# Optimization experiments

Measured on AMD Instinct MI355X. Metric: run time of the kernel, lower is better.

The kernel has to match this reference:

```python
import jax, jax.numpy as jnp
import numpy as np

NUM_SKILLS = 50000
HIDDEN = 64
B, T = 8192, 1024
EPS = 1e-6


def setup_inputs() -> dict:
    key = jax.random.key(0)
    ks = jax.random.split(key, 8)
    X = jax.random.randint(ks[0], (B,), 0, NUM_SKILLS)
    y = jax.random.randint(ks[1], (B, T), 0, 2, dtype=jnp.int32)
    embed = jax.random.normal(ks[2], (NUM_SKILLS, HIDDEN), jnp.float32)
    bound = 1.0 / np.sqrt(HIDDEN)
    W0 = jax.random.uniform(ks[3], (HIDDEN, HIDDEN), jnp.float32, -bound, bound)
    b0 = jnp.zeros((HIDDEN,), jnp.float32)
    W1 = jax.random.uniform(ks[4], (HIDDEN, HIDDEN), jnp.float32, -bound, bound)
    b1 = jnp.zeros((HIDDEN,), jnp.float32)
    Wout = jax.random.uniform(ks[5], (HIDDEN, 4), jnp.float32, -bound, bound)
    bout = jnp.zeros((4,), jnp.float32)
    return {"X": X, "y": y, "embed": embed, "W0": W0, "b0": b0,
            "W1": W1, "b1": b1, "Wout": Wout, "bout": bout}


def reference(X, y, embed, W0, b0, W1, b1, Wout, bout):
    # Per-student BKT params from embedding + 2-layer MLP + sigmoid, clamped
    h = embed[X]                                   # (B, H)
    h = jax.nn.relu(h @ W0 + b0)
    h = jax.nn.relu(h @ W1 + b1)
    params = jnp.clip(jax.nn.sigmoid(h @ Wout + bout), EPS, 1.0 - EPS)  # (B, 4)
    l, g, s, prior = params[:, 0], params[:, 1], params[:, 2], params[:, 3]

    def step(latent, y_t):
        true_correct = jnp.where(y_t == -1, 0, y_t)
        correct = latent * (1.0 - s) + (1.0 - latent) * g
        k_t1 = latent * (1.0 - s) / correct
        k_t0 = latent * s / (latent * s + (1.0 - latent) * (1.0 - g))
        k_t = jnp.where(true_correct > 0.5, k_t1, k_t0)
        next_latent = jnp.clip(k_t + (1.0 - k_t) * l, EPS, 1.0 - EPS)
        return next_latent, (correct, latent)

    _, (corrects, latents) = jax.lax.scan(step, prior, y.T)  # scan over T
    return corrects.T, latents.T                            # (B, T) each
```

## Files before the change

kernel.cpp:

```cpp
#include <hip/hip_runtime.h>

#define TSTEPS 1024
#define NROWS  8192
#define CLEN   16
#define KEPS   1e-6f

__device__ __forceinline__ float clampP(float x) {
    return fminf(fmaxf(x, KEPS), 1.f - KEPS);
}
__device__ __forceinline__ float sigm(float v) {
    return 1.0f / (1.0f + __expf(-v));
}

__global__ __launch_bounds__(256) void bkt_fused_v7(
    const int* __restrict__ X, const int* __restrict__ y,
    const float* __restrict__ embed,
    const float* __restrict__ W0, const float* __restrict__ b0,
    const float* __restrict__ W1, const float* __restrict__ b1,
    const float* __restrict__ Wout, const float* __restrict__ bout,
    float* __restrict__ out_corr, float* __restrict__ out_lat)
{
    const int lane = threadIdx.x & 63;
    const int wid  = threadIdx.x >> 6;
    const int row  = blockIdx.x * 4 + wid;

    __shared__ float hstage[4][64];
    __shared__ float trbuf[4][2][64 * 17];
    float* hbuf = hstage[wid];
    float* shc  = trbuf[wid][0];
    float* shl  = trbuf[wid][1];

    const int4* yrow = (const int4*)(y + (size_t)row * TSTEPS);
    const int4 vy0 = yrow[0 * 64 + lane];
    const int4 vy1 = yrow[1 * 64 + lane];
    const int4 vy2 = yrow[2 * 64 + lane];
    const int4 vy3 = yrow[3 * 64 + lane];

    const int skill = X[row];
    hbuf[lane] = embed[(size_t)skill * 64 + lane];
    float acc = b0[lane];
    #pragma unroll
    for (int k4 = 0; k4 < 16; ++k4) {
        const float4 e = *(const float4*)&hbuf[k4 * 4];
        acc = fmaf(e.x, W0[(k4 * 4 + 0) * 64 + lane], acc);
        acc = fmaf(e.y, W0[(k4 * 4 + 1) * 64 + lane], acc);
        acc = fmaf(e.z, W0[(k4 * 4 + 2) * 64 + lane], acc);
        acc = fmaf(e.w, W0[(k4 * 4 + 3) * 64 + lane], acc);
    }
    hbuf[lane] = fmaxf(acc, 0.f);
    acc = b1[lane];
    #pragma unroll
    for (int k4 = 0; k4 < 16; ++k4) {
        const float4 e = *(const float4*)&hbuf[k4 * 4];
        acc = fmaf(e.x, W1[(k4 * 4 + 0) * 64 + lane], acc);
        acc = fmaf(e.y, W1[(k4 * 4 + 1) * 64 + lane], acc);
        acc = fmaf(e.z, W1[(k4 * 4 + 2) * 64 + lane], acc);
        acc = fmaf(e.w, W1[(k4 * 4 + 3) * 64 + lane], acc);
    }
    const float h2 = fmaxf(acc, 0.f);

    const float4 wo = ((const float4*)Wout)[lane];
    float p0 = h2 * wo.x, p1 = h2 * wo.y, p2 = h2 * wo.z, p3 = h2 * wo.w;
    #pragma unroll
    for (int off = 32; off >= 1; off >>= 1) {
        p0 += __shfl_xor(p0, off, 64);
        p1 += __shfl_xor(p1, off, 64);
        p2 += __shfl_xor(p2, off, 64);
        p3 += __shfl_xor(p3, off, 64);
    }
    const float4 bo = *(const float4*)bout;
    const float l     = clampP(sigm(p0 + bo.x));
    const float g     = clampP(sigm(p1 + bo.y));
    const float s     = clampP(sigm(p2 + bo.z));
    const float prior = clampP(sigm(p3 + bo.w));

    unsigned long long B_[4][4];
    B_[0][0] = __ballot(vy0.x > 0); B_[0][1] = __ballot(vy0.y > 0);
    B_[0][2] = __ballot(vy0.z > 0); B_[0][3] = __ballot(vy0.w > 0);
    B_[1][0] = __ballot(vy1.x > 0); B_[1][1] = __ballot(vy1.y > 0);
    B_[1][2] = __ballot(vy1.z > 0); B_[1][3] = __ballot(vy1.w > 0);
    B_[2][0] = __ballot(vy2.x > 0); B_[2][1] = __ballot(vy2.y > 0);
    B_[2][2] = __ballot(vy2.z > 0); B_[2][3] = __ballot(vy2.w > 0);
    B_[3][0] = __ballot(vy3.x > 0); B_[3][1] = __ballot(vy3.y > 0);
    B_[3][2] = __ballot(vy3.z > 0); B_[3][3] = __ballot(vy3.w > 0);
    const int jsel  = lane >> 4;
    const int ibase = (lane & 15) * 4;
    unsigned msk = 0;
    #pragma unroll
    for (int e = 0; e < 4; ++e) {
        const unsigned long long be =
            (jsel == 0) ? B_[0][e] : (jsel == 1) ? B_[1][e] :
            (jsel == 2) ? B_[2][e] : B_[3][e];
        const unsigned n  = (unsigned)(be >> ibase) & 0xFu;
        const unsigned sp = (n & 1u) | ((n & 2u) << 3) | ((n & 4u) << 6) | ((n & 8u) << 9);
        msk |= sp << e;
    }

    const float c1 = 1.f - s - g, d1 = g;
    const float e00_1 = fmaf(l, c1, (1.f - l) * (1.f - s));
    const float e01_1 = l * d1;
    const float c0 = s + g - 1.f, d0 = 1.f - g;
    const float e00_0 = fmaf(l, c0, (1.f - l) * s);
    const float e01_0 = l * d0;

    float m00 = 1.f, m01 = 0.f, m10 = 0.f, m11 = 1.f;
    #pragma unroll
    for (int t = 0; t < CLEN; ++t) {
        const bool one = (msk >> t) & 1u;
        const float e00 = one ? e00_1 : e00_0;
        const float e01 = one ? e01_1 : e01_0;
        const float e10 = one ? c1 : c0;
        const float e11 = one ? d1 : d0;
        const float n00 = fmaf(e00, m00, e01 * m10);
        const float n01 = fmaf(e00, m01, e01 * m11);
        const float n10 = fmaf(e10, m00, e11 * m10);
        const float n11 = fmaf(e10, m01, e11 * m11);
        if ((t & 3) == 3) {
            const float inv = __builtin_amdgcn_rcpf(n11);
            m00 = n00 * inv; m01 = n01 * inv; m10 = n10 * inv; m11 = 1.f;
        } else {
            m00 = n00; m01 = n01; m10 = n10; m11 = n11;
        }
    }

    float s00 = m00, s01 = m01, s10 = m10, s11 = m11;
    #pragma unroll
    for (int d = 1; d < 64; d <<= 1) {
        const float t00 = __shfl_up(s00, d, 64);
        const float t01 = __shfl_up(s01, d, 64);
        const float t10 = __shfl_up(s10, d, 64);
        const float t11 = __shfl_up(s11, d, 64);
        if (lane >= d) {
            const float r00 = fmaf(s00, t00, s01 * t10);
            const float r01 = fmaf(s00, t01, s01 * t11);
            const float r10 = fmaf(s10, t00, s11 * t10);
            const float r11 = fmaf(s10, t01, s11 * t11);
            const float inv = __builtin_amdgcn_rcpf(r11);
            s00 = r00 * inv; s01 = r01 * inv; s10 = r10 * inv; s11 = 1.f;
        }
    }
    const float x00 = __shfl_up(s00, 1, 64);
    const float x01 = __shfl_up(s01, 1, 64);
    const float x10 = __shfl_up(s10, 1, 64);
    const float x11 = __shfl_up(s11, 1, 64);
    float L0;
    if (lane == 0) {
        L0 = prior;
    } else {
        const float num = fmaf(x00, prior, x01);
        const float den = fmaf(x10, prior, x11);
        L0 = clampP(num * __builtin_amdgcn_rcpf(den));
    }

    const float a   = 1.f - s;
    const float omg = 1.f - g;
    const float oml = 1.f - l;
    float Lc = L0;
    #pragma unroll
    for (int t = 0; t < CLEN; ++t) {
        const float correct = fmaf(Lc, c1, g);
        const float den0    = fmaf(Lc, c0, omg);
        shc[lane * 17 + t] = correct;
        shl[lane * 17 + t] = Lc;
        const bool one = (msk >> t) & 1u;
        const float den = one ? correct : den0;
        const float num = Lc * (one ? a : s);
        const float k   = num * __builtin_amdgcn_rcpf(den);
        Lc = clampP(fmaf(k, oml, l));
    }

    float* oc = out_corr + (size_t)row * TSTEPS;
    float* ol = out_lat  + (size_t)row * TSTEPS;
    #pragma unroll
    for (int j = 0; j < 4; ++j) {
        const int c    = j * 16 + (lane >> 2);
        const int q    = (lane & 3) * 4;
        const int base = c * 17 + q;
        float4 vc, vl;
        vc.x = shc[base + 0]; vc.y = shc[base + 1]; vc.z = shc[base + 2]; vc.w = shc[base + 3];
        vl.x = shl[base + 0]; vl.y = shl[base + 1]; vl.z = shl[base + 2]; vl.w = shl[base + 3];
        *(float4*)(oc + j * 256 + lane * 4) = vc;
        *(float4*)(ol + j * 256 + lane * 4) = vl;
    }
}

extern "C" void kernel_launch(void* const* d_in, const int* in_sizes, int n_in,
                              void* d_out, int out_size, void* d_ws, size_t ws_size,
                              hipStream_t stream) {
    const int*   X     = (const int*)  d_in[0];
    const int*   y     = (const int*)  d_in[1];
    const float* embed = (const float*)d_in[2];
    const float* W0    = (const float*)d_in[3];
    const float* b0    = (const float*)d_in[4];
    const float* W1    = (const float*)d_in[5];
    const float* b1    = (const float*)d_in[6];
    const float* Wout  = (const float*)d_in[7];
    const float* bout  = (const float*)d_in[8];

    float* out_corr = (float*)d_out;
    float* out_lat  = out_corr + (size_t)NROWS * TSTEPS;

    bkt_fused_v7<<<NROWS / 4, 256, 0, stream>>>(
        X, y, embed, W0, b0, W1, b1, Wout, bout, out_corr, out_lat);
}
```

Measured before the change: 121.7 us.

## Process two rows per wavefront to interleave independent scan chains

Each wavefront now handles two student rows instead of one. The two rows' MLP, matrix-product scan and recurrence steps are interleaved, which gives more instruction-level parallelism and hides the latency of the serial dependency chains. The W0/W1 weight loads are shared across both rows, and the grid is halved to match. In exchange, register pressure rises, the second row's outputs are buffered in registers before reusing the LDS transpose buffer, and there are half as many waves to hide memory latency.

```diff
diff --git a/kernel.cpp b/kernel.cpp
--- a/kernel.cpp
+++ b/kernel.cpp
@@ -12,7 +12,25 @@
     return 1.0f / (1.0f + __expf(-v));
 }
 
-__global__ __launch_bounds__(256) void bkt_fused_v7(
+__device__ __forceinline__ unsigned fold_msk(
+    const unsigned long long B0[4], const unsigned long long B1[4],
+    const unsigned long long B2[4], const unsigned long long B3[4],
+    int jsel, int ibase)
+{
+    unsigned msk = 0;
+    #pragma unroll
+    for (int e = 0; e < 4; ++e) {
+        const unsigned long long be =
+            (jsel == 0) ? B0[e] : (jsel == 1) ? B1[e] :
+            (jsel == 2) ? B2[e] : B3[e];
+        const unsigned n  = (unsigned)(be >> ibase) & 0xFu;
+        const unsigned sp = (n & 1u) | ((n & 2u) << 3) | ((n & 4u) << 6) | ((n & 8u) << 9);
+        msk |= sp << e;
+    }
+    return msk;
+}
+
+__global__ __launch_bounds__(256) void bkt_fused_v8(
     const int* __restrict__ X, const int* __restrict__ y,
     const float* __restrict__ embed,
     const float* __restrict__ W0, const float* __restrict__ b0,
@@ -22,155 +40,250 @@
 {
     const int lane = threadIdx.x & 63;
     const int wid  = threadIdx.x >> 6;
-    const int row  = blockIdx.x * 4 + wid;
-
-    __shared__ float hstage[4][64];
+    const int rowA = blockIdx.x * 8 + wid * 2;
+    const int rowB = rowA + 1;
+
+    __shared__ float hstage[4][2][64];
     __shared__ float trbuf[4][2][64 * 17];
-    float* hbuf = hstage[wid];
-    float* shc  = trbuf[wid][0];
-    float* shl  = trbuf[wid][1];
-
-    const int4* yrow = (const int4*)(y + (size_t)row * TSTEPS);
-    const int4 vy0 = yrow[0 * 64 + lane];
-    const int4 vy1 = yrow[1 * 64 + lane];
-    const int4 vy2 = yrow[2 * 64 + lane];
-    const int4 vy3 = yrow[3 * 64 + lane];
-
-    const int skill = X[row];
-    hbuf[lane] = embed[(size_t)skill * 64 + lane];
-    float acc = b0[lane];
-    #pragma unroll
-    for (int k4 = 0; k4 < 16; ++k4) {
-        const float4 e = *(const float4*)&hbuf[k4 * 4];
-        acc = fmaf(e.x, W0[(k4 * 4 + 0) * 64 + lane], acc);
-        acc = fmaf(e.y, W0[(k4 * 4 + 1) * 64 + lane], acc);
-        acc = fmaf(e.z, W0[(k4 * 4 + 2) * 64 + lane], acc);
-        acc = fmaf(e.w, W0[(k4 * 4 + 3) * 64 + lane], acc);
-    }
-    hbuf[lane] = fmaxf(acc, 0.f);
-    acc = b1[lane];
-    #pragma unroll
-    for (int k4 = 0; k4 < 16; ++k4) {
-        const float4 e = *(const float4*)&hbuf[k4 * 4];
-        acc = fmaf(e.x, W1[(k4 * 4 + 0) * 64 + lane], acc);
-        acc = fmaf(e.y, W1[(k4 * 4 + 1) * 64 + lane], acc);
-        acc = fmaf(e.z, W1[(k4 * 4 + 2) * 64 + lane], acc);
-        acc = fmaf(e.w, W1[(k4 * 4 + 3) * 64 + lane], acc);
-    }
-    const float h2 = fmaxf(acc, 0.f);
-
-    const float4 wo = ((const float4*)Wout)[lane];
-    float p0 = h2 * wo.x, p1 = h2 * wo.y, p2 = h2 * wo.z, p3 = h2 * wo.w;
-    #pragma unroll
-    for (int off = 32; off >= 1; off >>= 1) {
-        p0 += __shfl_xor(p0, off, 64);
-        p1 += __shfl_xor(p1, off, 64);
-        p2 += __shfl_xor(p2, off, 64);
-        p3 += __shfl_xor(p3, off, 64);
-    }
-    const float4 bo = *(const float4*)bout;
-    const float l     = clampP(sigm(p0 + bo.x));
-    const float g     = clampP(sigm(p1 + bo.y));
-    const float s     = clampP(sigm(p2 + bo.z));
-    const float prior = clampP(sigm(p3 + bo.w));
-
-    unsigned long long B_[4][4];
-    B_[0][0] = __ballot(vy0.x > 0); B_[0][1] = __ballot(vy0.y > 0);
-    B_[0][2] = __ballot(vy0.z > 0); B_[0][3] = __ballot(vy0.w > 0);
-    B_[1][0] = __ballot(vy1.x > 0); B_[1][1] = __ballot(vy1.y > 0);
-    B_[1][2] = __ballot(vy1.z > 0); B_[1][3] = __ballot(vy1.w > 0);
-    B_[2][0] = __ballot(vy2.x > 0); B_[2][1] = __ballot(vy2.y > 0);
-    B_[2][2] = __ballot(vy2.z > 0); B_[2][3] = __ballot(vy2.w > 0);
-    B_[3][0] = __ballot(vy3.x > 0); B_[3][1] = __ballot(vy3.y > 0);
-    B_[3][2] = __ballot(vy3.z > 0); B_[3][3] = __ballot(vy3.w > 0);
+    float* hA  = hstage[wid][0];
+    float* hB  = hstage[wid][1];
+    float* shc = trbuf[wid][0];
+    float* shl = trbuf[wid][1];
+
+    const int4* yA = (const int4*)(y + (size_t)rowA * TSTEPS);
+    const int4* yB = (const int4*)(y + (size_t)rowB * TSTEPS);
+    const int4 va0 = yA[0 * 64 + lane], va1 = yA[1 * 64 + lane];
+    const int4 va2 = yA[2 * 64 + lane], va3 = yA[3 * 64 + lane];
+    const int4 vb0 = yB[0 * 64 + lane], vb1 = yB[1 * 64 + lane];
+    const int4 vb2 = yB[2 * 64 + lane], vb3 = yB[3 * 64 + lane];
+
+    const int skA = X[rowA], skB = X[rowB];
+    const float emA = embed[(size_t)skA * 64 + lane];
+    const float emB = embed[(size_t)skB * 64 + lane];
+
     const int jsel  = lane >> 4;
     const int ibase = (lane & 15) * 4;
-    unsigned msk = 0;
-    #pragma unroll
-    for (int e = 0; e < 4; ++e) {
-        const unsigned long long be =
-            (jsel == 0) ? B_[0][e] : (jsel == 1) ? B_[1][e] :
-            (jsel == 2) ? B_[2][e] : B_[3][e];
-        const unsigned n  = (unsigned)(be >> ibase) & 0xFu;
-        const unsigned sp = (n & 1u) | ((n & 2u) << 3) | ((n & 4u) << 6) | ((n & 8u) << 9);
-        msk |= sp << e;
-    }
-
-    const float c1 = 1.f - s - g, d1 = g;
-    const float e00_1 = fmaf(l, c1, (1.f - l) * (1.f - s));
-    const float e01_1 = l * d1;
-    const float c0 = s + g - 1.f, d0 = 1.f - g;
-    const float e00_0 = fmaf(l, c0, (1.f - l) * s);
-    const float e01_0 = l * d0;
-
-    float m00 = 1.f, m01 = 0.f, m10 = 0.f, m11 = 1.f;
+    unsigned mskA, mskB;
+    {
+        unsigned long long A0[4] = { __ballot(va0.x > 0), __ballot(va0.y > 0),
+                                     __ballot(va0.z > 0), __ballot(va0.w > 0) };
+        unsigned long long A1[4] = { __ballot(va1.x > 0), __ballot(va1.y > 0),
+                                     __ballot(va1.z > 0), __ballot(va1.w > 0) };
+        unsigned long long A2[4] = { __ballot(va2.x > 0), __ballot(va2.y > 0),
+                                     __ballot(va2.z > 0), __ballot(va2.w > 0) };
+        unsigned long long A3[4] = { __ballot(va3.x > 0), __ballot(va3.y > 0),
+                                     __ballot(va3.z > 0), __ballot(va3.w > 0) };
+        mskA = fold_msk(A0, A1, A2, A3, jsel, ibase);
+    }
+    {
+        unsigned long long C0[4] = { __ballot(vb0.x > 0), __ballot(vb0.y > 0),
+                                     __ballot(vb0.z > 0), __ballot(vb0.w > 0) };
+        unsigned long long C1[4] = { __ballot(vb1.x > 0), __ballot(vb1.y > 0),
+                                     __ballot(vb1.z > 0), __ballot(vb1.w > 0) };
+        unsigned long long C2[4] = { __ballot(vb2.x > 0), __ballot(vb2.y > 0),
+                                     __ballot(vb2.z > 0), __ballot(vb2.w > 0) };
+        unsigned long long C3[4] = { __ballot(vb3.x > 0), __ballot(vb3.y > 0),
+                                     __ballot(vb3.z > 0), __ballot(vb3.w > 0) };
+        mskB = fold_msk(C0, C1, C2, C3, jsel, ibase);
+    }
+
+    hA[lane] = emA;
+    hB[lane] = emB;
+    float accA = b0[lane], accB = accA;
+    #pragma unroll
+    for (int k4 = 0; k4 < 16; ++k4) {
+        const float4 eA = *(const float4*)&hA[k4 * 4];
+        const float4 eB = *(const float4*)&hB[k4 * 4];
+        const float w0 = W0[(k4 * 4 + 0) * 64 + lane];
+        const float w1 = W0[(k4 * 4 + 1) * 64 + lane];
+        const float w2 = W0[(k4 * 4 + 2) * 64 + lane];
+        const float w3 = W0[(k4 * 4 + 3) * 64 + lane];
+        accA = fmaf(eA.x, w0, accA); accA = fmaf(eA.y, w1, accA);
+        accA = fmaf(eA.z, w2, accA); accA = fmaf(eA.w, w3, accA);
+        accB = fmaf(eB.x, w0, accB); accB = fmaf(eB.y, w1, accB);
+        accB = fmaf(eB.z, w2, accB); accB = fmaf(eB.w, w3, accB);
+    }
+    hA[lane] = fmaxf(accA, 0.f);
+    hB[lane] = fmaxf(accB, 0.f);
+    accA = b1[lane]; accB = accA;
+    #pragma unroll
+    for (int k4 = 0; k4 < 16; ++k4) {
+        const float4 eA = *(const float4*)&hA[k4 * 4];
+        const float4 eB = *(const float4*)&hB[k4 * 4];
+        const float w0 = W1[(k4 * 4 + 0) * 64 + lane];
+        const float w1 = W1[(k4 * 4 + 1) * 64 + lane];
+        const float w2 = W1[(k4 * 4 + 2) * 64 + lane];
+        const float w3 = W1[(k4 * 4 + 3) * 64 + lane];
+        accA = fmaf(eA.x, w0, accA); accA = fmaf(eA.y, w1, accA);
+        accA = fmaf(eA.z, w2, accA); accA = fmaf(eA.w, w3, accA);
+        accB = fmaf(eB.x, w0, accB); accB = fmaf(eB.y, w1, accB);
+        accB = fmaf(eB.z, w2, accB); accB = fmaf(eB.w, w3, accB);
+    }
+    const float h2A = fmaxf(accA, 0.f);
+    const float h2B = fmaxf(accB, 0.f);
+
+    const float4 wo = ((const float4*)Wout)[lane];
+    float pA0 = h2A * wo.x, pA1 = h2A * wo.y, pA2 = h2A * wo.z, pA3 = h2A * wo.w;
+    float pB0 = h2B * wo.x, pB1 = h2B * wo.y, pB2 = h2B * wo.z, pB3 = h2B * wo.w;
+    #pragma unroll
+    for (int off = 32; off >= 1; off >>= 1) {
+        pA0 += __shfl_xor(pA0, off, 64);
+        pA1 += __shfl_xor(pA1, off, 64);
+        pA2 += __shfl_xor(pA2, off, 64);
+        pA3 += __shfl_xor(pA3, off, 64);
+        pB0 += __shfl_xor(pB0, off, 64);
+        pB1 += __shfl_xor(pB1, off, 64);
+        pB2 += __shfl_xor(pB2, off, 64);
+        pB3 += __shfl_xor(pB3, off, 64);
+    }
+    const float4 bo = *(const float4*)bout;
+    const float lA     = clampP(sigm(pA0 + bo.x));
+    const float gA     = clampP(sigm(pA1 + bo.y));
+    const float sA     = clampP(sigm(pA2 + bo.z));
+    const float priorA = clampP(sigm(pA3 + bo.w));
+    const float lB     = clampP(sigm(pB0 + bo.x));
+    const float gB     = clampP(sigm(pB1 + bo.y));
+    const float sB     = clampP(sigm(pB2 + bo.z));
+    const float priorB = clampP(sigm(pB3 + bo.w));
+
+    const float c1A = 1.f - sA - gA, d1A = gA;
+    const float e00_1A = fmaf(lA, c1A, (1.f - lA) * (1.f - sA));
+    const float e01_1A = lA * d1A;
+    const float c0A = sA + gA - 1.f, d0A = 1.f - gA;
+    const float e00_0A = fmaf(lA, c0A, (1.f - lA) * sA);
+    const float e01_0A = lA * d0A;
+
+    const float c1B = 1.f - sB - gB, d1B = gB;
+    const float e00_1B = fmaf(lB, c1B, (1.f - lB) * (1.f - sB));
+    const float e01_1B = lB * d1B;
+    const float c0B = sB + gB - 1.f, d0B = 1.f - gB;
+    const float e00_0B = fmaf(lB, c0B, (1.f - lB) * sB);
+    const float e01_0B = lB * d0B;
+
+    float mA00 = 1.f, mA01 = 0.f, mA10 = 0.f, mA11 = 1.f;
+    float mB00 = 1.f, mB01 = 0.f, mB10 = 0.f, mB11 = 1.f;
     #pragma unroll
     for (int t = 0; t < CLEN; ++t) {
-        const bool one = (msk >> t) & 1u;
-        const float e00 = one ? e00_1 : e00_0;
-        const float e01 = one ? e01_1 : e01_0;
-        const float e10 = one ? c1 : c0;
-        const float e11 = one ? d1 : d0;
-        const float n00 = fmaf(e00, m00, e01 * m10);
-        const float n01 = fmaf(e00, m01, e01 * m11);
-        const float n10 = fmaf(e10, m00, e11 * m10);
-        const float n11 = fmaf(e10, m01, e11 * m11);
-        if ((t & 3) == 3) {
-            const float inv = __builtin_amdgcn_rcpf(n11);
-            m00 = n00 * inv; m01 = n01 * inv; m10 = n10 * inv; m11 = 1.f;
-        } else {
-            m00 = n00; m01 = n01; m10 = n10; m11 = n11;
-        }
-    }
-
-    float s00 = m00, s01 = m01, s10 = m10, s11 = m11;
+        {
+            const bool one = (mskA >> t) & 1u;
+            const float e00 = one ? e00_1A : e00_0A;
+            const float e01 = one ? e01_1A : e01_0A;
+            const float e10 = one ? c1A : c0A;
+            const float e11 = one ? d1A : d0A;
+            const float n00 = fmaf(e00, mA00, e01 * mA10);
+            const float n01 = fmaf(e00, mA01, e01 * mA11);
+            const float n10 = fmaf(e10, mA00, e11 * mA10);
+            const float n11 = fmaf(e10, mA01, e11 * mA11);
+            if ((t & 3) == 3) {
+                const float inv = __builtin_amdgcn_rcpf(n11);
+                mA00 = n00 * inv; mA01 = n01 * inv; mA10 = n10 * inv; mA11 = 1.f;
+            } else {
+                mA00 = n00; mA01 = n01; mA10 = n10; mA11 = n11;
+            }
+        }
+        {
+            const bool one = (mskB >> t) & 1u;
+            const float e00 = one ? e00_1B : e00_0B;
+            const float e01 = one ? e01_1B : e01_0B;
+            const float e10 = one ? c1B : c0B;
+            const float e11 = one ? d1B : d0B;
+            const float n00 = fmaf(e00, mB00, e01 * mB10);
+            const float n01 = fmaf(e00, mB01, e01 * mB11);
+            const float n10 = fmaf(e10, mB00, e11 * mB10);
+            const float n11 = fmaf(e10, mB01, e11 * mB11);
+            if ((t & 3) == 3) {
+                const float inv = __builtin_amdgcn_rcpf(n11);
+                mB00 = n00 * inv; mB01 = n01 * inv; mB10 = n10 * inv; mB11 = 1.f;
+            } else {
+                mB00 = n00; mB01 = n01; mB10 = n10; mB11 = n11;
+            }
+        }
+    }
+
+    float sA00 = mA00, sA01 = mA01, sA10 = mA10, sA11 = mA11;
+    float sB00 = mB00, sB01 = mB01, sB10 = mB10, sB11 = mB11;
     #pragma unroll
     for (int d = 1; d < 64; d <<= 1) {
-        const float t00 = __shfl_up(s00, d, 64);
-        const float t01 = __shfl_up(s01, d, 64);
-        const float t10 = __shfl_up(s10, d, 64);
-        const float t11 = __shfl_up(s11, d, 64);
+        const float tA00 = __shfl_up(sA00, d, 64);
+        const float tA01 = __shfl_up(sA01, d, 64);
+        const float tA10 = __shfl_up(sA10, d, 64);
+        const float tA11 = __shfl_up(sA11, d, 64);
+        const float tB00 = __shfl_up(sB00, d, 64);
+        const float tB01 = __shfl_up(sB01, d, 64);
+        const float tB10 = __shfl_up(sB10, d, 64);
+        const float tB11 = __shfl_up(sB11, d, 64);
         if (lane >= d) {
-            const float r00 = fmaf(s00, t00, s01 * t10);
-            const float r01 = fmaf(s00, t01, s01 * t11);
-            const float r10 = fmaf(s10, t00, s11 * t10);
-            const float r11 = fmaf(s10, t01, s11 * t11);
-            const float inv = __builtin_amdgcn_rcpf(r11);
-            s00 = r00 * inv; s01 = r01 * inv; s10 = r10 * inv; s11 = 1.f;
-        }
-    }
-    const float x00 = __shfl_up(s00, 1, 64);
-    const float x01 = __shfl_up(s01, 1, 64);
-    const float x10 = __shfl_up(s10, 1, 64);
-    const float x11 = __shfl_up(s11, 1, 64);
-    float L0;
+            {
+                const float r00 = fmaf(sA00, tA00, sA01 * tA10);
+                const float r01 = fmaf(sA00, tA01, sA01 * tA11);
+                const float r10 = fmaf(sA10, tA00, sA11 * tA10);
+                const float r11 = fmaf(sA10, tA01, sA11 * tA11);
+                const float inv = __builtin_amdgcn_rcpf(r11);
+                sA00 = r00 * inv; sA01 = r01 * inv; sA10 = r10 * inv; sA11 = 1.f;
+            }
+            {
+                const float r00 = fmaf(sB00, tB00, sB01 * tB10);
+                const float r01 = fmaf(sB00, tB01, sB01 * tB11);
+                const float r10 = fmaf(sB10, tB00, sB11 * tB10);
+                const float r11 = fmaf(sB10, tB01, sB11 * tB11);
+                const float inv = __builtin_amdgcn_rcpf(r11);
+                sB00 = r00 * inv; sB01 = r01 * inv; sB10 = r10 * inv; sB11 = 1.f;
+            }
+        }
+    }
+    const float xA00 = __shfl_up(sA00, 1, 64);
+    const float xA01 = __shfl_up(sA01, 1, 64);
+    const float xA10 = __shfl_up(sA10, 1, 64);
+    const float xA11 = __shfl_up(sA11, 1, 64);
+    const float xB00 = __shfl_up(sB00, 1, 64);
+    const float xB01 = __shfl_up(sB01, 1, 64);
+    const float xB10 = __shfl_up(sB10, 1, 64);
+    const float xB11 = __shfl_up(sB11, 1, 64);
+    float L0A, L0B;
     if (lane == 0) {
-        L0 = prior;
+        L0A = priorA;
+        L0B = priorB;
     } else {
-        const float num = fmaf(x00, prior, x01);
-        const float den = fmaf(x10, prior, x11);
-        L0 = clampP(num * __builtin_amdgcn_rcpf(den));
-    }
-
-    const float a   = 1.f - s;
-    const float omg = 1.f - g;
-    const float oml = 1.f - l;
-    float Lc = L0;
+        const float numA = fmaf(xA00, priorA, xA01);
+        const float denA = fmaf(xA10, priorA, xA11);
+        L0A = clampP(numA * __builtin_amdgcn_rcpf(denA));
+        const float numB = fmaf(xB00, priorB, xB01);
+        const float denB = fmaf(xB10, priorB, xB11);
+        L0B = clampP(numB * __builtin_amdgcn_rcpf(denB));
+    }
+
+    const float aA = 1.f - sA, omgA = 1.f - gA, omlA = 1.f - lA;
+    const float aB = 1.f - sB, omgB = 1.f - gB, omlB = 1.f - lB;
+    float crB[CLEN], ltB[CLEN];
+    float LcA = L0A, LcB = L0B;
     #pragma unroll
     for (int t = 0; t < CLEN; ++t) {
-        const float correct = fmaf(Lc, c1, g);
-        const float den0    = fmaf(Lc, c0, omg);
-        shc[lane * 17 + t] = correct;
-        shl[lane * 17 + t] = Lc;
-        const bool one = (msk >> t) & 1u;
-        const float den = one ? correct : den0;
-        const float num = Lc * (one ? a : s);
-        const float k   = num * __builtin_amdgcn_rcpf(den);
-        Lc = clampP(fmaf(k, oml, l));
-    }
-
-    float* oc = out_corr + (size_t)row * TSTEPS;
-    float* ol = out_lat  + (size_t)row * TSTEPS;
+        {
+            const float correct = fmaf(LcA, c1A, gA);
+            const float den0    = fmaf(LcA, c0A, omgA);
+            shc[lane * 17 + t] = correct;
+            shl[lane * 17 + t] = LcA;
+            const bool one = (mskA >> t) & 1u;
+            const float den = one ? correct : den0;
+            const float num = LcA * (one ? aA : sA);
+            const float k   = num * __builtin_amdgcn_rcpf(den);
+            LcA = clampP(fmaf(k, omlA, lA));
+        }
+        {
+            const float correct = fmaf(LcB, c1B, gB);
+            const float den0    = fmaf(LcB, c0B, omgB);
+            crB[t] = correct;
+            ltB[t] = LcB;
+            const bool one = (mskB >> t) & 1u;
+            const float den = one ? correct : den0;
+            const float num = LcB * (one ? aB : sB);
+            const float k   = num * __builtin_amdgcn_rcpf(den);
+            LcB = clampP(fmaf(k, omlB, lB));
+        }
+    }
+
+    float* ocA = out_corr + (size_t)rowA * TSTEPS;
+    float* olA = out_lat  + (size_t)rowA * TSTEPS;
     #pragma unroll
     for (int j = 0; j < 4; ++j) {
         const int c    = j * 16 + (lane >> 2);
@@ -179,8 +292,27 @@
         float4 vc, vl;
         vc.x = shc[base + 0]; vc.y = shc[base + 1]; vc.z = shc[base + 2]; vc.w = shc[base + 3];
         vl.x = shl[base + 0]; vl.y = shl[base + 1]; vl.z = shl[base + 2]; vl.w = shl[base + 3];
-        *(float4*)(oc + j * 256 + lane * 4) = vc;
-        *(float4*)(ol + j * 256 + lane * 4) = vl;
+        *(float4*)(ocA + j * 256 + lane * 4) = vc;
+        *(float4*)(olA + j * 256 + lane * 4) = vl;
+    }
+
+    #pragma unroll
+    for (int t = 0; t < CLEN; ++t) {
+        shc[lane * 17 + t] = crB[t];
+        shl[lane * 17 + t] = ltB[t];
+    }
+    float* ocB = out_corr + (size_t)rowB * TSTEPS;
+    float* olB = out_lat  + (size_t)rowB * TSTEPS;
+    #pragma unroll
+    for (int j = 0; j < 4; ++j) {
+        const int c    = j * 16 + (lane >> 2);
+        const int q    = (lane & 3) * 4;
+        const int base = c * 17 + q;
+        float4 vc, vl;
+        vc.x = shc[base + 0]; vc.y = shc[base + 1]; vc.z = shc[base + 2]; vc.w = shc[base + 3];
+        vl.x = shl[base + 0]; vl.y = shl[base + 1]; vl.z = shl[base + 2]; vl.w = shl[base + 3];
+        *(float4*)(ocB + j * 256 + lane * 4) = vc;
+        *(float4*)(olB + j * 256 + lane * 4) = vl;
     }
 }
 
@@ -200,6 +332,6 @@
     float* out_corr = (float*)d_out;
     float* out_lat  = out_corr + (size_t)NROWS * TSTEPS;
 
-    bkt_fused_v7<<<NROWS / 4, 256, 0, stream>>>(
+    bkt_fused_v8<<<NROWS / 8, 256, 0, stream>>>(
         X, y, embed, W0, b0, W1, b1, Wout, bout, out_corr, out_lat);
 }
```

Measured after the change: 119.6 us, median of 2. Within noise of the previous version (-1.8%).
